# Optimization experiments

Measured on AMD Instinct MI355X. Metric: run time of the kernel, lower is better.

## Reference

```python
import jax, jax.numpy as jnp
import numpy as np

N_NODES = 50000
N_EDGES = 800000
F_IN = 128
HEADS = 4
HEAD_DIM = 32  # hidden_size // heads
HIDDEN = HEADS * HEAD_DIM
N_GRAPHS = 64
LEAKY_SLOPE = 0.01
EPS_LN = 1e-5


def setup_inputs() -> dict:
    key = jax.random.key(0)
    ks = jax.random.split(key, 12)
    x = jax.random.normal(ks[0], (N_NODES, F_IN), dtype=jnp.float32)
    edge_index = jax.random.randint(ks[1], (2, N_EDGES), 0, N_NODES, dtype=jnp.int64)
    batch = jnp.sort(jax.random.randint(ks[2], (N_NODES,), 0, N_GRAPHS, dtype=jnp.int64))
    s = 1.0 / np.sqrt(F_IN).astype(np.float32)
    Wq = jax.random.normal(ks[3], (F_IN, HIDDEN), dtype=jnp.float32) * s
    bq = jnp.zeros((HIDDEN,), jnp.float32)
    Wk = jax.random.normal(ks[4], (F_IN, HIDDEN), dtype=jnp.float32) * s
    bk = jnp.zeros((HIDDEN,), jnp.float32)
    Wv = jax.random.normal(ks[5], (F_IN, HIDDEN), dtype=jnp.float32) * s
    bv = jnp.zeros((HIDDEN,), jnp.float32)
    Ws = jax.random.normal(ks[6], (F_IN, HIDDEN), dtype=jnp.float32) * s  # root/skip lin
    bs = jnp.zeros((HIDDEN,), jnp.float32)
    ln_w = jnp.ones((HIDDEN,), jnp.float32)
    ln_b = jnp.zeros((HIDDEN,), jnp.float32)
    return {"x": x, "edge_index": edge_index, "batch": batch,
            "Wq": Wq, "bq": bq, "Wk": Wk, "bk": bk, "Wv": Wv, "bv": bv,
            "Ws": Ws, "bs": bs, "ln_w": ln_w, "ln_b": ln_b}


def reference(x, edge_index, batch, Wq, bq, Wk, bk, Wv, bv, Ws, bs, ln_w, ln_b):
    N = x.shape[0]
    src, dst = edge_index[0], edge_index[1]  # message j(src) -> i(dst)
    q = (x @ Wq + bq).reshape(N, HEADS, HEAD_DIM)
    k = (x @ Wk + bk).reshape(N, HEADS, HEAD_DIM)
    v = (x @ Wv + bv).reshape(N, HEADS, HEAD_DIM)
    # per-edge attention logits [E, H]
    alpha = jnp.einsum('ehc,ehc->eh', q[dst], k[src]) / jnp.sqrt(jnp.float32(HEAD_DIM))
    # scatter-softmax over incoming edges of each destination node
    m = jax.ops.segment_max(alpha, dst, num_segments=N)
    m = jnp.where(jnp.isfinite(m), m, 0.0)  # empty segments -> -inf; neutralize
    ex = jnp.exp(alpha - m[dst])
    denom = jax.ops.segment_sum(ex, dst, num_segments=N)
    attn = ex / (denom[dst] + 1e-16)
    # scatter-add aggregation of weighted values, concat heads
    out = jax.ops.segment_sum(attn[:, :, None] * v[src], dst, num_segments=N)
    out = out.reshape(N, HIDDEN) + x @ Ws + bs  # root/skip connection
    # PyG graph-mode LayerNorm: normalize over all nodes+channels of each graph
    cnt = jax.ops.segment_sum(jnp.ones((N,), out.dtype), batch, num_segments=N_GRAPHS)
    norm = jnp.maximum(cnt, 1.0) * HIDDEN
    mean = jax.ops.segment_sum(out.sum(-1), batch, num_segments=N_GRAPHS) / norm
    outc = out - mean[batch][:, None]
    var = jax.ops.segment_sum((outc * outc).sum(-1), batch, num_segments=N_GRAPHS) / norm
    y = outc / jnp.sqrt(var + EPS_LN)[batch][:, None]
    y = y * ln_w + ln_b
    y = jnp.where(y > 0, y, LEAKY_SLOPE * y)  # LeakyReLU
    return (y, attn)
```

## Files before the change

kernel.cpp:

```cpp
#include <hip/hip_runtime.h>
#include <hip/hip_fp16.h>

constexpr int N_NODES = 50000;
constexpr int N_EDGES = 800000;
constexpr int HIDDEN  = 128;
constexpr float RSQRT_D = 0.17677669529663687f;
constexpr int Y_SIZE = N_NODES * HIDDEN;
constexpr int M_PAD  = 50048;
constexpr int MM_BLOCKS = M_PAD / 128;
constexpr int SCAN_BLOCKS = 196;
constexpr int XCVT_BLOCKS = (M_PAD * 16) / 256;
constexpr int HIST_BLOCKS = N_EDGES / 256;
constexpr int STAT_BLOCKS = (N_NODES + 31) / 32;
constexpr int EX_CAP = 128;

constexpr size_t OFF_Q      = 0;
constexpr size_t OFF_K      = 6400000;
constexpr size_t OFF_S      = 19200000;
constexpr size_t OFF_EXC    = 22400000;
constexpr size_t OFF_WT     = 25600000;
constexpr size_t OFF_GSUM   = 25800000;
constexpr size_t OFF_GSQ    = 25800064;
constexpr size_t OFF_GCNT   = 25800128;
constexpr size_t OFF_DEG    = 25800192;
constexpr size_t OFF_OFFS   = 25850192;
constexpr size_t OFF_CURSOR = 25900224;
constexpr size_t OFF_CSR    = 25950224;
constexpr size_t OFF_PART   = 27550224;

typedef __attribute__((ext_vector_type(8))) short bf16x8;
typedef __attribute__((ext_vector_type(4))) float f32x4;

__device__ __forceinline__ short f2bf(float f) {
    unsigned u = __float_as_uint(f);
    unsigned r = (u + 0x7fff + ((u >> 16) & 1)) >> 16;
    return (short)r;
}

__device__ __forceinline__ void gload_lds16(const void* g, void* l) {
    __builtin_amdgcn_global_load_lds(
        (const __attribute__((address_space(1))) void*)g,
        (__attribute__((address_space(3))) void*)l, 16, 0, 0);
}

__global__ __launch_bounds__(256) void k_prep(
    const float* __restrict__ x,
    const float* __restrict__ Wq, const float* __restrict__ Wk,
    const float* __restrict__ Wv, const float* __restrict__ Wsm,
    const int* __restrict__ dst,
    short* __restrict__ xs, short* __restrict__ wt, int* __restrict__ deg)
{
    int b = blockIdx.x;
    if (b < XCVT_BLOCKS) {
        int tid = b * 256 + threadIdx.x;
        int row = tid >> 4, ci = tid & 15;
        short o[8];
        if (row < N_NODES) {
            float4 a = *(const float4*)&x[(size_t)row * 128 + ci * 8];
            float4 bb = *(const float4*)&x[(size_t)row * 128 + ci * 8 + 4];
            o[0] = f2bf(a.x); o[1] = f2bf(a.y); o[2] = f2bf(a.z); o[3] = f2bf(a.w);
            o[4] = f2bf(bb.x); o[5] = f2bf(bb.y); o[6] = f2bf(bb.z); o[7] = f2bf(bb.w);
        } else {
            #pragma unroll
            for (int j = 0; j < 8; ++j) o[j] = 0;
        }
        int cs = ci ^ (row & 7);
        *(int4*)&xs[(size_t)row * 128 + cs * 8] = *(int4*)o;
    } else if (b < XCVT_BLOCKS + 32) {
        int tid = (b - XCVT_BLOCKS) * 256 + threadIdx.x;
        int mat = tid >> 11, n = (tid >> 4) & 127, kg = tid & 15;
        const float* W = (mat == 0) ? Wq : (mat == 1) ? Wk : (mat == 2) ? Wv : Wsm;
        short o[8];
        #pragma unroll
        for (int j = 0; j < 8; ++j) o[j] = f2bf(W[(kg * 8 + j) * 128 + n]);
        int cs = kg ^ (n & 7);
        *(int4*)&wt[mat * 16384 + n * 128 + cs * 8] = *(int4*)o;
    } else {
        int e = (b - XCVT_BLOCKS - 32) * 256 + threadIdx.x;
        atomicAdd(&deg[dst[e]], 1);
    }
}

__global__ __launch_bounds__(256) void k_mmscan(
    const short* __restrict__ xs, const short* __restrict__ wt,
    const float* __restrict__ bq, const float* __restrict__ bk,
    const float* __restrict__ bv, const float* __restrict__ bs,
    __half* __restrict__ qb, __half* __restrict__ kv, __half* __restrict__ sb,
    const int* __restrict__ deg, int* __restrict__ part)
{
    if (blockIdx.x >= MM_BLOCKS) {
        const int t = threadIdx.x;
        int idx = (blockIdx.x - MM_BLOCKS) * 256 + t;
        int v = (idx < N_NODES) ? deg[idx] : 0;
        #pragma unroll
        for (int o = 1; o < 64; o <<= 1) v += __shfl_xor(v, o);
        __shared__ int wsum1[4];
        if ((t & 63) == 0) wsum1[t >> 6] = v;
        __syncthreads();
        if (t == 0) part[blockIdx.x - MM_BLOCKS] = wsum1[0] + wsum1[1] + wsum1[2] + wsum1[3];
        return;
    }
    __shared__ __align__(16) char As[32768];
    __shared__ __align__(16) char Bs[32768];
    const int t = threadIdx.x, lane = t & 63, wv = t >> 6;
    const int m0 = blockIdx.x * 128;
    const int wm = wv >> 1, wn = wv & 1;

    const char* gA = (const char*)xs + (size_t)m0 * 256;
    #pragma unroll
    for (int i = 0; i < 8; ++i) {
        int chunk = wv * 8 + i;
        gload_lds16(gA + chunk * 1024 + lane * 16, As + chunk * 1024);
        gload_lds16((const char*)wt + chunk * 1024 + lane * 16, Bs + chunk * 1024);
    }
    __syncthreads();

    bf16x8 af[4][4];
    #pragma unroll
    for (int ks = 0; ks < 4; ++ks) {
        const int cbase = ks * 64 + ((lane >> 4) << 4);
        #pragma unroll
        for (int mf = 0; mf < 4; ++mf) {
            int mr = wm * 64 + mf * 16 + (lane & 15);
            af[ks][mf] = *(const bf16x8*)(As + mr * 256 + (cbase ^ ((mr & 7) << 4)));
        }
    }

    const float* Bbs[4] = {bq, bk, bv, bs};
    #pragma unroll
    for (int mat = 0; mat < 4; ++mat) {
        f32x4 acc[4][4];
        #pragma unroll
        for (int nf = 0; nf < 4; ++nf) {
            float bc = Bbs[mat][wn * 64 + nf * 16 + (lane & 15)];
            #pragma unroll
            for (int mf = 0; mf < 4; ++mf) acc[mf][nf] = (f32x4){bc, bc, bc, bc};
        }
        #pragma unroll
        for (int ks = 0; ks < 4; ++ks) {
            bf16x8 bfr[4];
            const int cbase = ks * 64 + ((lane >> 4) << 4);
            #pragma unroll
            for (int nf = 0; nf < 4; ++nf) {
                int nc = wn * 64 + nf * 16 + (lane & 15);
                bfr[nf] = *(const bf16x8*)(Bs + nc * 256 + (cbase ^ ((nc & 7) << 4)));
            }
            #pragma unroll
            for (int mf = 0; mf < 4; ++mf)
                #pragma unroll
                for (int nf = 0; nf < 4; ++nf)
                    acc[mf][nf] = __builtin_amdgcn_mfma_f32_16x16x32_bf16(
                        af[ks][mf], bfr[nf], acc[mf][nf], 0, 0, 0);
        }
        __syncthreads();
        if (mat < 3) {
            const char* gB = (const char*)wt + (mat + 1) * 32768;
            #pragma unroll
            for (int i = 0; i < 8; ++i) {
                int chunk = wv * 8 + i;
                gload_lds16(gB + chunk * 1024 + lane * 16, Bs + chunk * 1024);
            }
        }
        __half* base = (mat == 0) ? qb : (mat == 1) ? kv : (mat == 2) ? (kv + 128) : sb;
        const int rs = (mat == 1 || mat == 2) ? 256 : 128;
        const int colbase = wn * 64 + (lane & 15);
        #pragma unroll
        for (int mf = 0; mf < 4; ++mf) {
            int rowb = m0 + wm * 64 + mf * 16 + ((lane >> 4) << 2);
            #pragma unroll
            for (int nf = 0; nf < 4; ++nf) {
                int col = colbase + nf * 16;
                #pragma unroll
                for (int r = 0; r < 4; ++r) {
                    int node = rowb + r;
                    if (node < N_NODES)
                        base[(size_t)node * rs + col] = __float2half_rn(acc[mf][nf][r]);
                }
            }
        }
        __syncthreads();
    }
}

__global__ __launch_bounds__(256) void k_scan3(const int* __restrict__ deg,
                                               const int* __restrict__ part,
                                               int* __restrict__ offs,
                                               int* __restrict__ cursor)
{
    __shared__ int pbuf[256];
    __shared__ int wsum[4];
    const int t = threadIdx.x;
    int pv = (t < SCAN_BLOCKS) ? part[t] : 0;
    pbuf[t] = pv;
    __syncthreads();
    for (int o = 1; o < 256; o <<= 1) {
        int tmp = (t >= o) ? pbuf[t - o] : 0;
        __syncthreads();
        pbuf[t] += tmp;
        __syncthreads();
    }
    const int bbase = (blockIdx.x == 0) ? 0 : pbuf[blockIdx.x - 1];

    const int idx = blockIdx.x * 256 + t;
    const int lane = t & 63, w = t >> 6;
    int v = (idx < N_NODES) ? deg[idx] : 0;
    int inc = v;
    #pragma unroll
    for (int o = 1; o < 64; o <<= 1) {
        int nb = __shfl_up(inc, o);
        if (lane >= o) inc += nb;
    }
    if (lane == 63) wsum[w] = inc;
    __syncthreads();
    int wbase = 0;
    #pragma unroll
    for (int i = 0; i < 4; ++i) if (i < w) wbase += wsum[i];
    int excl = bbase + wbase + inc - v;
    if (idx < N_NODES) {
        offs[idx] = excl;
        cursor[idx] = excl;
    }
    if (idx == 0) offs[N_NODES] = N_EDGES;
}

__global__ __launch_bounds__(256) void k_scatter(
    const int* __restrict__ src, const int* __restrict__ dst,
    int* __restrict__ cursor, int2* __restrict__ csr)
{
    int e = blockIdx.x * 256 + threadIdx.x;
    int d = dst[e];
    int p = atomicAdd(&cursor[d], 1);
    csr[p] = make_int2(src[e], e);
}

#define GRP_COMPUTE(BASE, K0, K1, K2, K3, V0, V1, V2, V3)                     \
    {                                                                         \
        float2 f0 = __half22float2(K0), f1 = __half22float2(K1),              \
               f2 = __half22float2(K2), f3 = __half22float2(K3);              \
        float p = qf[0].x*f0.x + qf[0].y*f0.y + qf[1].x*f1.x + qf[1].y*f1.y   \
                + qf[2].x*f2.x + qf[2].y*f2.y + qf[3].x*f3.x + qf[3].y*f3.y;  \
        p += __shfl_xor(p, 1);                                                \
        p += __shfl_xor(p, 2);                                                \
        const float ex = __expf(p * RSQRT_D);                                 \
        dsum += ex;                                                           \
        float2 g0 = __half22float2(V0), g1 = __half22float2(V1),              \
               g2 = __half22float2(V2), g3 = __half22float2(V3);              \
        acc[0] += ex * g0.x; acc[1] += ex * g0.y;                             \
        acc[2] += ex * g1.x; acc[3] += ex * g1.y;                             \
        acc[4] += ex * g2.x; acc[5] += ex * g2.y;                             \
        acc[6] += ex * g3.x; acc[7] += ex * g3.y;                             \
        if ((lane & 3) == 0) {                                                \
            int sl = (BASE) + qtr - begin;                                    \
            if (sl < EX_CAP) exs[nl][sl * 4 + h] = ex;                        \
            else             exc[((size_t)((BASE) + qtr)) * 4 + h] = ex;      \
        }                                                                     \
    }

__global__ __launch_bounds__(256) void k_fused(
    const __half* __restrict__ qb, const __half* __restrict__ kv,
    const __half* __restrict__ sb,
    const int* __restrict__ offs, const int2* __restrict__ csr,
    float* __restrict__ exc, float* __restrict__ attn,
    float* __restrict__ outb)
{
    __shared__ __align__(16) float exs[4][EX_CAP * 4];
    const int t = threadIdx.x;
    const int lane = t & 63;
    const int nl = t >> 6;
    const int n = blockIdx.x * 4 + nl;
    const int begin = offs[n], end = offs[n + 1];
    const int cl  = lane & 15;
    const int qtr = lane >> 4;
    const int h   = cl >> 2;

    const __half2* qp = (const __half2*)(qb + (size_t)n * 128 + cl * 8);
    float2 qf[4];
    #pragma unroll
    for (int j = 0; j < 4; ++j) qf[j] = __half22float2(qp[j]);

    float acc[8] = {0.f, 0.f, 0.f, 0.f, 0.f, 0.f, 0.f, 0.f};
    float dsum = 0.f;
    int i = begin;

    if (i + 4 <= end) {
        const __half2* kpC = (const __half2*)(kv + (size_t)csr[i + qtr].x * 256 + cl * 8);
        __half2 kC0 = kpC[0],  kC1 = kpC[1],  kC2 = kpC[2],  kC3 = kpC[3];
        __half2 vC0 = kpC[64], vC1 = kpC[65], vC2 = kpC[66], vC3 = kpC[67];
        while (i + 8 <= end) {
            const __half2* kpN = (const __half2*)(kv + (size_t)csr[i + 4 + qtr].x * 256 + cl * 8);
            __half2 kN0 = kpN[0],  kN1 = kpN[1],  kN2 = kpN[2],  kN3 = kpN[3];
            __half2 vN0 = kpN[64], vN1 = kpN[65], vN2 = kpN[66], vN3 = kpN[67];
            GRP_COMPUTE(i, kC0, kC1, kC2, kC3, vC0, vC1, vC2, vC3);
            kC0 = kN0; kC1 = kN1; kC2 = kN2; kC3 = kN3;
            vC0 = vN0; vC1 = vN1; vC2 = vN2; vC3 = vN3;
            i += 4;
        }
        GRP_COMPUTE(i, kC0, kC1, kC2, kC3, vC0, vC1, vC2, vC3);
        i += 4;
    }
    if (i < end) {
        const int eIdx = i + qtr;
        const bool act = eIdx < end;
        const __half2* kp = (const __half2*)(kv + (size_t)csr[act ? eIdx : end - 1].x * 256 + cl * 8);
        __half2 ka0 = kp[0],  ka1 = kp[1],  ka2 = kp[2],  ka3 = kp[3];
        __half2 va0 = kp[64], va1 = kp[65], va2 = kp[66], va3 = kp[67];
        float2 f0 = __half22float2(ka0), f1 = __half22float2(ka1),
               f2 = __half22float2(ka2), f3 = __half22float2(ka3);
        float p = qf[0].x*f0.x + qf[0].y*f0.y + qf[1].x*f1.x + qf[1].y*f1.y
                + qf[2].x*f2.x + qf[2].y*f2.y + qf[3].x*f3.x + qf[3].y*f3.y;
        p += __shfl_xor(p, 1);
        p += __shfl_xor(p, 2);
        const float ex = act ? __expf(p * RSQRT_D) : 0.f;
        dsum += ex;
        float2 g0 = __half22float2(va0), g1 = __half22float2(va1),
               g2 = __half22float2(va2), g3 = __half22float2(va3);
        acc[0] += ex * g0.x; acc[1] += ex * g0.y;
        acc[2] += ex * g1.x; acc[3] += ex * g1.y;
        acc[4] += ex * g2.x; acc[5] += ex * g2.y;
        acc[6] += ex * g3.x; acc[7] += ex * g3.y;
        if (((lane & 3) == 0) && act) {
            int sl = eIdx - begin;
            if (sl < EX_CAP) exs[nl][sl * 4 + h] = ex;
            else             exc[(size_t)eIdx * 4 + h] = ex;
        }
    }

    dsum += __shfl_xor(dsum, 16);
    dsum += __shfl_xor(dsum, 32);
    #pragma unroll
    for (int j = 0; j < 8; ++j) {
        acc[j] += __shfl_xor(acc[j], 16);
        acc[j] += __shfl_xor(acc[j], 32);
    }
    const float rd0 = 1.f / (__shfl(dsum, 0)  + 1e-16f);
    const float rd1 = 1.f / (__shfl(dsum, 4)  + 1e-16f);
    const float rd2 = 1.f / (__shfl(dsum, 8)  + 1e-16f);
    const float rd3 = 1.f / (__shfl(dsum, 12) + 1e-16f);

    if (lane < 16) {
        const float rdn = 1.f / (dsum + 1e-16f);
        const __half2* sp = (const __half2*)(sb + (size_t)n * 128 + cl * 8);
        float o[8];
        #pragma unroll
        for (int j = 0; j < 4; ++j) {
            float2 sf = __half22float2(sp[j]);
            o[2*j]   = acc[2*j]   * rdn + sf.x;
            o[2*j+1] = acc[2*j+1] * rdn + sf.y;
        }
        *(float4*)&outb[(size_t)n * 128 + cl * 8]     = make_float4(o[0], o[1], o[2], o[3]);
        *(float4*)&outb[(size_t)n * 128 + cl * 8 + 4] = make_float4(o[4], o[5], o[6], o[7]);
    }

    __builtin_amdgcn_sched_barrier(0);

    for (int slot = begin + lane; slot < end; slot += 64) {
        const int eid = csr[slot].y;
        const int sl = slot - begin;
        float4 e4 = (sl < EX_CAP) ? *(const float4*)&exs[nl][sl * 4]
                                  : *(const float4*)&exc[(size_t)slot * 4];
        ((float4*)attn)[eid] = make_float4(e4.x * rd0, e4.y * rd1,
                                           e4.z * rd2, e4.w * rd3);
    }
}

__global__ __launch_bounds__(256) void k_stats(
    const float* __restrict__ out, const int* __restrict__ batch,
    float* __restrict__ gsum, float* __restrict__ gsq, int* __restrict__ gcnt)
{
    __shared__ float nsum[32], nsq[32];
    __shared__ int   ngr[32];
    const int t = threadIdx.x;
    const int nl = t >> 3, part = t & 7;
    const int n = blockIdx.x * 32 + nl;
    float lsum = 0.f, lsq = 0.f;
    if (n < N_NODES) {
        size_t base = (size_t)n * 128 + part * 16;
        #pragma unroll
        for (int i = 0; i < 4; ++i) {
            float4 o = *(const float4*)&out[base + i * 4];
            lsum += o.x + o.y + o.z + o.w;
            lsq  += o.x * o.x + o.y * o.y + o.z * o.z + o.w * o.w;
        }
    }
    #pragma unroll
    for (int o = 1; o < 8; o <<= 1) {
        lsum += __shfl_xor(lsum, o);
        lsq  += __shfl_xor(lsq, o);
    }
    if (part == 0) { nsum[nl] = lsum; nsq[nl] = lsq; ngr[nl] = (n < N_NODES) ? batch[n] : -1; }
    __syncthreads();
    if (t == 0) {
        float acc = 0.f, accq = 0.f; int cg = ngr[0], cnt = 0;
        for (int i = 0; i < 32; ++i) {
            int g = ngr[i];
            if (g != cg) {
                if (cg >= 0) { atomicAdd(&gsum[cg], acc); atomicAdd(&gsq[cg], accq);
                               atomicAdd(&gcnt[cg], cnt); }
                acc = 0.f; accq = 0.f; cnt = 0; cg = g;
            }
            acc += nsum[i]; accq += nsq[i]; ++cnt;
        }
        if (cg >= 0) { atomicAdd(&gsum[cg], acc); atomicAdd(&gsq[cg], accq);
                       atomicAdd(&gcnt[cg], cnt); }
    }
}

__global__ __launch_bounds__(256) void k_final(
    const float* __restrict__ out, const int* __restrict__ batch,
    const float* __restrict__ gsum, const float* __restrict__ gsq,
    const int* __restrict__ gcnt,
    const float* __restrict__ lnw, const float* __restrict__ lnb,
    float* __restrict__ y)
{
    int idx = blockIdx.x * 256 + threadIdx.x;
    int n = idx >> 7, c = idx & 127;
    int g = batch[n];
    float norm = fmaxf((float)gcnt[g], 1.f) * 128.f;
    float mean = gsum[g] / norm;
    float var  = gsq[g] / norm - mean * mean;
    float inv  = rsqrtf(var + 1e-5f);
    float val  = (out[idx] - mean) * inv * lnw[c] + lnb[c];
    y[idx] = val > 0.f ? val : 0.01f * val;
}

extern "C" void kernel_launch(void* const* d_in, const int* in_sizes, int n_in,
                              void* d_out, int out_size, void* d_ws, size_t ws_size,
                              hipStream_t stream)
{
    (void)in_sizes; (void)n_in; (void)out_size; (void)ws_size;
    const float* x    = (const float*)d_in[0];
    const int*   ei   = (const int*)  d_in[1];
    const int*   batch= (const int*)  d_in[2];
    const float* Wq   = (const float*)d_in[3];
    const float* bq   = (const float*)d_in[4];
    const float* Wk   = (const float*)d_in[5];
    const float* bk   = (const float*)d_in[6];
    const float* Wv   = (const float*)d_in[7];
    const float* bv   = (const float*)d_in[8];
    const float* Wsm  = (const float*)d_in[9];
    const float* bs   = (const float*)d_in[10];
    const float* lnw  = (const float*)d_in[11];
    const float* lnb  = (const float*)d_in[12];

    float* outp = (float*)d_out;
    float* ws   = (float*)d_ws;

    const int* srcI = ei;
    const int* dstI = ei + N_EDGES;

    __half* qb      = (__half*)(ws + OFF_Q);
    __half* kv      = (__half*)(ws + OFF_K);
    __half* sb      = (__half*)(ws + OFF_S);
    float*  exc     = ws + OFF_EXC;
    short*  wt      = (short*)(ws + OFF_WT);
    float*  gsum    = ws + OFF_GSUM;
    float*  gsq     = ws + OFF_GSQ;
    int*    gcnt    = (int*)(ws + OFF_GCNT);
    int*    deg     = (int*)(ws + OFF_DEG);
    int*    offs    = (int*)(ws + OFF_OFFS);
    int*    cursor  = (int*)(ws + OFF_CURSOR);
    int2*   csr     = (int2*)(ws + OFF_CSR);
    int*    partArr = (int*)(ws + OFF_PART);

    float* outb  = outp;
    short* x_swz = (short*)outp;
    float* attn  = outp + Y_SIZE;

    hipMemsetAsync(gsum, 0, (size_t)(192 + N_NODES) * sizeof(float), stream);

    k_prep<<<XCVT_BLOCKS + 32 + HIST_BLOCKS, 256, 0, stream>>>(
        x, Wq, Wk, Wv, Wsm, dstI, x_swz, wt, deg);
    k_mmscan<<<MM_BLOCKS + SCAN_BLOCKS, 256, 0, stream>>>(
        x_swz, wt, bq, bk, bv, bs, qb, kv, sb, deg, partArr);
    k_scan3<<<SCAN_BLOCKS, 256, 0, stream>>>(deg, partArr, offs, cursor);
    k_scatter<<<N_EDGES / 256, 256, 0, stream>>>(srcI, dstI, cursor, csr);
    k_fused<<<N_NODES / 4, 256, 0, stream>>>(qb, kv, sb, offs, csr,
                                             exc, attn, outb);
    k_stats<<<STAT_BLOCKS, 256, 0, stream>>>(outb, batch, gsum, gsq, gcnt);
    k_final<<<Y_SIZE / 256, 256, 0, stream>>>(outb, batch, gsum, gsq, gcnt,
                                              lnw, lnb, outp);
}
```

Baseline: 228.0 us.

## Fuse per-node LayerNorm stats into attention kernel, use fdot2, vectorize final

The attention kernel now computes each node's output sum and sum of squares and writes them to a small per-node array. This lets the stats kernel read 8 bytes per node instead of re-reading the full 128-float output row. The q·k dot product uses the packed fp16 fdot2 builtin instead of converting to fp32 first, which can change rounding slightly. The final normalisation kernel processes float4 per thread, launching a quarter as many threads.

New measurement: 224.4 us. No clear change (-1.6%).

```diff
diff --git a/kernel.cpp b/kernel.cpp
--- a/kernel.cpp
+++ b/kernel.cpp
@@ -11,7 +11,6 @@
 constexpr int SCAN_BLOCKS = 196;
 constexpr int XCVT_BLOCKS = (M_PAD * 16) / 256;
 constexpr int HIST_BLOCKS = N_EDGES / 256;
-constexpr int STAT_BLOCKS = (N_NODES + 31) / 32;
 constexpr int EX_CAP = 128;
 
 constexpr size_t OFF_Q      = 0;
@@ -27,9 +26,36 @@
 constexpr size_t OFF_CURSOR = 25900224;
 constexpr size_t OFF_CSR    = 25950224;
 constexpr size_t OFF_PART   = 27550224;
+constexpr size_t OFF_NSTAT  = 27550420;
 
 typedef __attribute__((ext_vector_type(8))) short bf16x8;
 typedef __attribute__((ext_vector_type(4))) float f32x4;
+typedef __attribute__((ext_vector_type(2))) _Float16 h2;
+
+#if defined(__has_builtin)
+# if __has_builtin(__builtin_amdgcn_fdot2)
+#  define HAS_FDOT2 1
+# endif
+#endif
+
+__device__ __forceinline__ float dot8(h2 a0, h2 a1, h2 a2, h2 a3,
+                                      h2 b0, h2 b1, h2 b2, h2 b3)
+{
+#ifdef HAS_FDOT2
+    float p = __builtin_amdgcn_fdot2(a0, b0, 0.f, false);
+    p = __builtin_amdgcn_fdot2(a1, b1, p, false);
+    p = __builtin_amdgcn_fdot2(a2, b2, p, false);
+    p = __builtin_amdgcn_fdot2(a3, b3, p, false);
+    return p;
+#else
+    float p = 0.f;
+    p += (float)a0.x * (float)b0.x + (float)a0.y * (float)b0.y;
+    p += (float)a1.x * (float)b1.x + (float)a1.y * (float)b1.y;
+    p += (float)a2.x * (float)b2.x + (float)a2.y * (float)b2.y;
+    p += (float)a3.x * (float)b3.x + (float)a3.y * (float)b3.y;
+    return p;
+#endif
+}
 
 __device__ __forceinline__ short f2bf(float f) {
     unsigned u = __float_as_uint(f);
@@ -235,10 +261,7 @@
 
 #define GRP_COMPUTE(BASE, K0, K1, K2, K3, V0, V1, V2, V3)                     \
     {                                                                         \
-        float2 f0 = __half22float2(K0), f1 = __half22float2(K1),              \
-               f2 = __half22float2(K2), f3 = __half22float2(K3);              \
-        float p = qf[0].x*f0.x + qf[0].y*f0.y + qf[1].x*f1.x + qf[1].y*f1.y   \
-                + qf[2].x*f2.x + qf[2].y*f2.y + qf[3].x*f3.x + qf[3].y*f3.y;  \
+        float p = dot8(K0, K1, K2, K3, qh0, qh1, qh2, qh3);                   \
         p += __shfl_xor(p, 1);                                                \
         p += __shfl_xor(p, 2);                                                \
         const float ex = __expf(p * RSQRT_D);                                 \
@@ -261,7 +284,7 @@
     const __half* __restrict__ sb,
     const int* __restrict__ offs, const int2* __restrict__ csr,
     float* __restrict__ exc, float* __restrict__ attn,
-    float* __restrict__ outb)
+    float* __restrict__ outb, float2* __restrict__ nstat)
 {
     __shared__ __align__(16) float exs[4][EX_CAP * 4];
     const int t = threadIdx.x;
@@ -273,23 +296,25 @@
     const int qtr = lane >> 4;
     const int h   = cl >> 2;
 
-    const __half2* qp = (const __half2*)(qb + (size_t)n * 128 + cl * 8);
-    float2 qf[4];
-    #pragma unroll
-    for (int j = 0; j < 4; ++j) qf[j] = __half22float2(qp[j]);
+    const h2* qp = (const h2*)(qb + (size_t)n * 128 + cl * 8);
+    const h2 qh0 = qp[0], qh1 = qp[1], qh2 = qp[2], qh3 = qp[3];
 
     float acc[8] = {0.f, 0.f, 0.f, 0.f, 0.f, 0.f, 0.f, 0.f};
     float dsum = 0.f;
     int i = begin;
 
     if (i + 4 <= end) {
-        const __half2* kpC = (const __half2*)(kv + (size_t)csr[i + qtr].x * 256 + cl * 8);
-        __half2 kC0 = kpC[0],  kC1 = kpC[1],  kC2 = kpC[2],  kC3 = kpC[3];
-        __half2 vC0 = kpC[64], vC1 = kpC[65], vC2 = kpC[66], vC3 = kpC[67];
+        const __half* rC = kv + (size_t)csr[i + qtr].x * 256 + cl * 8;
+        h2 kC0 = ((const h2*)rC)[0], kC1 = ((const h2*)rC)[1],
+           kC2 = ((const h2*)rC)[2], kC3 = ((const h2*)rC)[3];
+        __half2 vC0 = ((const __half2*)rC)[64], vC1 = ((const __half2*)rC)[65],
+                vC2 = ((const __half2*)rC)[66], vC3 = ((const __half2*)rC)[67];
         while (i + 8 <= end) {
-            const __half2* kpN = (const __half2*)(kv + (size_t)csr[i + 4 + qtr].x * 256 + cl * 8);
-            __half2 kN0 = kpN[0],  kN1 = kpN[1],  kN2 = kpN[2],  kN3 = kpN[3];
-            __half2 vN0 = kpN[64], vN1 = kpN[65], vN2 = kpN[66], vN3 = kpN[67];
+            const __half* rN = kv + (size_t)csr[i + 4 + qtr].x * 256 + cl * 8;
+            h2 kN0 = ((const h2*)rN)[0], kN1 = ((const h2*)rN)[1],
+               kN2 = ((const h2*)rN)[2], kN3 = ((const h2*)rN)[3];
+            __half2 vN0 = ((const __half2*)rN)[64], vN1 = ((const __half2*)rN)[65],
+                    vN2 = ((const __half2*)rN)[66], vN3 = ((const __half2*)rN)[67];
             GRP_COMPUTE(i, kC0, kC1, kC2, kC3, vC0, vC1, vC2, vC3);
             kC0 = kN0; kC1 = kN1; kC2 = kN2; kC3 = kN3;
             vC0 = vN0; vC1 = vN1; vC2 = vN2; vC3 = vN3;
@@ -301,13 +326,12 @@
     if (i < end) {
         const int eIdx = i + qtr;
         const bool act = eIdx < end;
-        const __half2* kp = (const __half2*)(kv + (size_t)csr[act ? eIdx : end - 1].x * 256 + cl * 8);
-        __half2 ka0 = kp[0],  ka1 = kp[1],  ka2 = kp[2],  ka3 = kp[3];
-        __half2 va0 = kp[64], va1 = kp[65], va2 = kp[66], va3 = kp[67];
-        float2 f0 = __half22float2(ka0), f1 = __half22float2(ka1),
-               f2 = __half22float2(ka2), f3 = __half22float2(ka3);
-        float p = qf[0].x*f0.x + qf[0].y*f0.y + qf[1].x*f1.x + qf[1].y*f1.y
-                + qf[2].x*f2.x + qf[2].y*f2.y + qf[3].x*f3.x + qf[3].y*f3.y;
+        const __half* rT = kv + (size_t)csr[act ? eIdx : end - 1].x * 256 + cl * 8;
+        h2 ka0 = ((const h2*)rT)[0], ka1 = ((const h2*)rT)[1],
+           ka2 = ((const h2*)rT)[2], ka3 = ((const h2*)rT)[3];
+        __half2 va0 = ((const __half2*)rT)[64], va1 = ((const __half2*)rT)[65],
+                va2 = ((const __half2*)rT)[66], va3 = ((const __half2*)rT)[67];
+        float p = dot8(ka0, ka1, ka2, ka3, qh0, qh1, qh2, qh3);
         p += __shfl_xor(p, 1);
         p += __shfl_xor(p, 2);
         const float ex = act ? __expf(p * RSQRT_D) : 0.f;
@@ -349,6 +373,14 @@
         }
         *(float4*)&outb[(size_t)n * 128 + cl * 8]     = make_float4(o[0], o[1], o[2], o[3]);
         *(float4*)&outb[(size_t)n * 128 + cl * 8 + 4] = make_float4(o[4], o[5], o[6], o[7]);
+        float lsum = o[0]+o[1]+o[2]+o[3]+o[4]+o[5]+o[6]+o[7];
+        float lsq  = o[0]*o[0]+o[1]*o[1]+o[2]*o[2]+o[3]*o[3]
+                   + o[4]*o[4]+o[5]*o[5]+o[6]*o[6]+o[7]*o[7];
+        lsum += __shfl_xor(lsum, 1); lsq += __shfl_xor(lsq, 1);
+        lsum += __shfl_xor(lsum, 2); lsq += __shfl_xor(lsq, 2);
+        lsum += __shfl_xor(lsum, 4); lsq += __shfl_xor(lsq, 4);
+        lsum += __shfl_xor(lsum, 8); lsq += __shfl_xor(lsq, 8);
+        if (lane == 0) nstat[n] = make_float2(lsum, lsq);
     }
 
     __builtin_amdgcn_sched_barrier(0);
@@ -364,41 +396,26 @@
 }
 
 __global__ __launch_bounds__(256) void k_stats(
-    const float* __restrict__ out, const int* __restrict__ batch,
+    const float2* __restrict__ nstat, const int* __restrict__ batch,
     float* __restrict__ gsum, float* __restrict__ gsq, int* __restrict__ gcnt)
 {
-    __shared__ float nsum[32], nsq[32];
-    __shared__ int   ngr[32];
+    __shared__ float ss[256], qq[256];
+    __shared__ int   gg[256];
     const int t = threadIdx.x;
-    const int nl = t >> 3, part = t & 7;
-    const int n = blockIdx.x * 32 + nl;
-    float lsum = 0.f, lsq = 0.f;
-    if (n < N_NODES) {
-        size_t base = (size_t)n * 128 + part * 16;
-        #pragma unroll
-        for (int i = 0; i < 4; ++i) {
-            float4 o = *(const float4*)&out[base + i * 4];
-            lsum += o.x + o.y + o.z + o.w;
-            lsq  += o.x * o.x + o.y * o.y + o.z * o.z + o.w * o.w;
-        }
-    }
-    #pragma unroll
-    for (int o = 1; o < 8; o <<= 1) {
-        lsum += __shfl_xor(lsum, o);
-        lsq  += __shfl_xor(lsq, o);
-    }
-    if (part == 0) { nsum[nl] = lsum; nsq[nl] = lsq; ngr[nl] = (n < N_NODES) ? batch[n] : -1; }
+    const int n = blockIdx.x * 256 + t;
+    float2 st = (n < N_NODES) ? nstat[n] : make_float2(0.f, 0.f);
+    ss[t] = st.x; qq[t] = st.y; gg[t] = (n < N_NODES) ? batch[n] : -1;
     __syncthreads();
     if (t == 0) {
-        float acc = 0.f, accq = 0.f; int cg = ngr[0], cnt = 0;
-        for (int i = 0; i < 32; ++i) {
-            int g = ngr[i];
+        float acc = 0.f, accq = 0.f; int cg = gg[0], cnt = 0;
+        for (int i = 0; i < 256; ++i) {
+            int g = gg[i];
             if (g != cg) {
                 if (cg >= 0) { atomicAdd(&gsum[cg], acc); atomicAdd(&gsq[cg], accq);
                                atomicAdd(&gcnt[cg], cnt); }
                 acc = 0.f; accq = 0.f; cnt = 0; cg = g;
             }
-            acc += nsum[i]; accq += nsq[i]; ++cnt;
+            acc += ss[i]; accq += qq[i]; ++cnt;
         }
         if (cg >= 0) { atomicAdd(&gsum[cg], acc); atomicAdd(&gsq[cg], accq);
                        atomicAdd(&gcnt[cg], cnt); }
@@ -413,14 +430,25 @@
     float* __restrict__ y)
 {
     int idx = blockIdx.x * 256 + threadIdx.x;
-    int n = idx >> 7, c = idx & 127;
+    int n = idx >> 5, c4 = idx & 31;
     int g = batch[n];
     float norm = fmaxf((float)gcnt[g], 1.f) * 128.f;
     float mean = gsum[g] / norm;
     float var  = gsq[g] / norm - mean * mean;
     float inv  = rsqrtf(var + 1e-5f);
-    float val  = (out[idx] - mean) * inv * lnw[c] + lnb[c];
-    y[idx] = val > 0.f ? val : 0.01f * val;
+    float4 o = *(const float4*)&out[(size_t)idx * 4];
+    float4 w = *(const float4*)&lnw[c4 * 4];
+    float4 b = *(const float4*)&lnb[c4 * 4];
+    float4 r;
+    r.x = (o.x - mean) * inv * w.x + b.x;
+    r.y = (o.y - mean) * inv * w.y + b.y;
+    r.z = (o.z - mean) * inv * w.z + b.z;
+    r.w = (o.w - mean) * inv * w.w + b.w;
+    r.x = r.x > 0.f ? r.x : 0.01f * r.x;
+    r.y = r.y > 0.f ? r.y : 0.01f * r.y;
+    r.z = r.z > 0.f ? r.z : 0.01f * r.z;
+    r.w = r.w > 0.f ? r.w : 0.01f * r.w;
+    *(float4*)&y[(size_t)idx * 4] = r;
 }
 
 extern "C" void kernel_launch(void* const* d_in, const int* in_sizes, int n_in,
@@ -461,6 +489,7 @@
     int*    cursor  = (int*)(ws + OFF_CURSOR);
     int2*   csr     = (int2*)(ws + OFF_CSR);
     int*    partArr = (int*)(ws + OFF_PART);
+    float2* nstat   = (float2*)(ws + OFF_NSTAT);
 
     float* outb  = outp;
     short* x_swz = (short*)outp;
@@ -475,8 +504,8 @@
     k_scan3<<<SCAN_BLOCKS, 256, 0, stream>>>(deg, partArr, offs, cursor);
     k_scatter<<<N_EDGES / 256, 256, 0, stream>>>(srcI, dstI, cursor, csr);
     k_fused<<<N_NODES / 4, 256, 0, stream>>>(qb, kv, sb, offs, csr,
-                                             exc, attn, outb);
-    k_stats<<<STAT_BLOCKS, 256, 0, stream>>>(outb, batch, gsum, gsq, gcnt);
-    k_final<<<Y_SIZE / 256, 256, 0, stream>>>(outb, batch, gsum, gsq, gcnt,
-                                              lnw, lnb, outp);
-}
+                                             exc, attn, outb, nstat);
+    k_stats<<<SCAN_BLOCKS, 256, 0, stream>>>(nstat, batch, gsum, gsq, gcnt);
+    k_final<<<Y_SIZE / 4 / 256, 256, 0, stream>>>(outb, batch, gsum, gsq, gcnt,
+                                                  lnw, lnb, outp);
+}
```
